# Optimization experiments

Hardware: AMD Instinct MI355X
Metric: run time of the kernel (lower is better)

## Reference

```python
import jax, jax.numpy as jnp
import numpy as np
from jax import lax

DISP = 4   # max displacement for correlation -> 81 channels
KSZ = 3    # deform/gate conv kernel size


def conv2d(x, w, b=None):
    out = lax.conv_general_dilated(x, w, (1, 1), 'SAME',
                                   dimension_numbers=('NCHW', 'OIHW', 'NCHW'))
    if b is not None:
        out = out + b[None, :, None, None]
    return out


def correlation(x1, x2, d=DISP):
    # FlowNet-style cost volume, kernel_size=1: per-displacement channel-mean dot product.
    B, C, H, W = x1.shape
    x2p = jnp.pad(x2, ((0, 0), (0, 0), (d, d), (d, d)))
    outs = []
    for dy in range(2 * d + 1):
        for dx in range(2 * d + 1):
            shifted = lax.dynamic_slice(x2p, (0, 0, dy, dx), (B, C, H, W))
            outs.append(jnp.sum(x1 * shifted, axis=1) / C)
    return jnp.stack(outs, axis=1)  # [B, (2d+1)^2, H, W]


def bilinear_sample(img, y, x):
    # img: [B,C,H,W]; y,x: [B,H,W] float sample coords; zero padding outside.
    B, C, H, W = img.shape
    y0 = jnp.floor(y); x0 = jnp.floor(x)
    y1 = y0 + 1.0;     x1 = x0 + 1.0
    wy1 = y - y0; wx1 = x - x0
    wy0 = 1.0 - wy1; wx0 = 1.0 - wx1
    flat = img.reshape(B, C, H * W)

    def gather(yi, xi):
        valid = (yi >= 0) & (yi <= H - 1) & (xi >= 0) & (xi <= W - 1)
        yc = jnp.clip(yi, 0, H - 1).astype(jnp.int32)
        xc = jnp.clip(xi, 0, W - 1).astype(jnp.int32)
        idx = (yc * W + xc).reshape(B, 1, H * W)
        g = jnp.take_along_axis(flat, idx, axis=2).reshape(B, C, H, W)
        return g * valid.astype(img.dtype)[:, None]

    return (gather(y0, x0) * (wy0 * wx0)[:, None]
          + gather(y0, x1) * (wy0 * wx1)[:, None]
          + gather(y1, x0) * (wy1 * wx0)[:, None]
          + gather(y1, x1) * (wy1 * wx1)[:, None])


def deform_conv(img, offset, w, k=KSZ):
    # offset: [B, 2*k*k, H, W] with (dy, dx) pairs per kernel tap (row-major).
    B, C, H, W = img.shape
    pad = (k - 1) // 2
    ys = jnp.arange(H, dtype=img.dtype)[None, :, None]
    xs = jnp.arange(W, dtype=img.dtype)[None, None, :]
    out = jnp.zeros((B, w.shape[0], H, W), dtype=img.dtype)
    for kk in range(k * k):
        ky, kx = kk // k, kk % k
        y = ys + (ky - pad) + offset[:, 2 * kk]
        x = xs + (kx - pad) + offset[:, 2 * kk + 1]
        s = bilinear_sample(img, y, x)
        out = out + jnp.einsum('oc,bchw->bohw', w[:, :, ky, kx], s)
    return out


def linear_scale(x, std_multiplier=3.0):
    pos = x > 0
    cnt = jnp.sum(pos).astype(x.dtype)
    mean = jnp.sum(jnp.where(pos, x, 0.0)) / jnp.maximum(cnt, 1.0)
    var = jnp.sum(jnp.where(pos, (x - mean) ** 2, 0.0)) / jnp.maximum(cnt - 1.0, 1.0)
    ub = mean + std_multiplier * jnp.sqrt(var)
    ub = jnp.where(cnt >= 2.0, ub, 1.0)  # matches torch nan / empty-positive fallback
    return jnp.clip(x, 0.0, lax.stop_gradient(ub)) / ub


def setup_inputs() -> dict:
    key = jax.random.key(0)
    ks = jax.random.split(key, 10)
    B, C, H, W = 8, 256, 64, 64
    f = jnp.float32
    inp = {
        'inputs':   jax.random.normal(ks[0], (B, C, H, W), f),
        'in_state': jax.random.normal(ks[1], (B, C, H, W), f),
        'w_reset':  jax.random.normal(ks[2], (C, 2 * C, 3, 3), f) * 0.02,
        'b_reset':  jnp.zeros((C,), f),
        'w_update': jax.random.normal(ks[3], (C, 2 * C, 3, 3), f) * 0.02,
        'b_update': jnp.zeros((C,), f),
        'w_out':    jax.random.normal(ks[4], (C, 2 * C, 3, 3), f) * 0.02,
        'b_out':    jnp.zeros((C,), f),
        'w_offset': jax.random.normal(ks[5], (18, 81, 1, 1), f) * 0.01,
        'w_align':  jax.random.normal(ks[6], (C, C, 3, 3), f) * 0.01,
    }
    return inp


def reference(inputs, in_state, w_reset, b_reset, w_update, b_update,
              w_out, b_out, w_offset, w_align):
    # align_features: correlation -> 1x1 offset conv -> deformable conv
    corr = correlation(inputs, in_state)
    offset = conv2d(corr, w_offset)
    aligned = deform_conv(in_state, offset, w_align)
    # ConvGRU gates with linear-scaled relu gates
    stacked = jnp.concatenate([inputs, aligned], axis=1)
    update = linear_scale(jax.nn.relu(conv2d(stacked, w_update, b_update)))
    reset = linear_scale(jax.nn.relu(conv2d(stacked, w_reset, b_reset)))
    out_in = jax.nn.relu(conv2d(jnp.concatenate([inputs, in_state * reset], axis=1), w_out, b_out))
    new_state = in_state * (1.0 - update) + out_in * update
    return (new_state, new_state)  # (out_feat, new_state)
```

## Files before the change

### kernel.cpp

```cpp
#include <hip/hip_runtime.h>
#include <stdint.h>
#include <math.h>

typedef unsigned short u16;
typedef short bf16x8 __attribute__((ext_vector_type(8)));
typedef float f32x4 __attribute__((ext_vector_type(4)));

#define MFMA16x16x32(a,b,c) __builtin_amdgcn_mfma_f32_16x16x32_bf16((a),(b),(c),0,0,0)

typedef __attribute__((address_space(3))) void as3_void;
typedef const __attribute__((address_space(1))) void as1_void;

__device__ __forceinline__ void g2l16(const void* g, void* l){
#if __has_builtin(__builtin_amdgcn_global_load_lds)
  __builtin_amdgcn_global_load_lds((as1_void*)g, (as3_void*)l, 16, 0, 0);
#else
  *(int4*)l = *(const int4*)g;
#endif
}

__device__ __forceinline__ u16 f2bf(float f){
  uint32_t u = __builtin_bit_cast(uint32_t, f);
  u += 0x7fffu + ((u >> 16) & 1u);
  return (u16)(u >> 16);
}
__device__ __forceinline__ float bf2f(u16 h){
  uint32_t u = ((uint32_t)h) << 16;
  return __builtin_bit_cast(float, u);
}
__device__ __forceinline__ void unpack8(int4 v, float* o){
  uint32_t w0=(uint32_t)v.x, w1=(uint32_t)v.y, w2=(uint32_t)v.z, w3=(uint32_t)v.w;
  o[0]=__builtin_bit_cast(float, w0<<16); o[1]=__builtin_bit_cast(float, w0&0xffff0000u);
  o[2]=__builtin_bit_cast(float, w1<<16); o[3]=__builtin_bit_cast(float, w1&0xffff0000u);
  o[4]=__builtin_bit_cast(float, w2<<16); o[5]=__builtin_bit_cast(float, w2&0xffff0000u);
  o[6]=__builtin_bit_cast(float, w3<<16); o[7]=__builtin_bit_cast(float, w3&0xffff0000u);
}
__device__ __forceinline__ int iclampi(int v,int lo,int hi){ return v<lo?lo:(v>hi?hi:v); }

__global__ void k_repack(const float* __restrict__ w_reset, const float* __restrict__ b_reset,
                         const float* __restrict__ w_update, const float* __restrict__ b_update,
                         const float* __restrict__ w_out, const float* __restrict__ w_offset,
                         const float* __restrict__ w_align,
                         u16* __restrict__ wgate, u16* __restrict__ wout,
                         u16* __restrict__ walign, float* __restrict__ woff,
                         float* __restrict__ biascat){
  int idx = blockIdx.x * 256 + threadIdx.x;
  if (idx < 512*4608){
    int e = idx & 7, j = (idx >> 3) & 2047, chunk = idx >> 14;
    int nb = chunk & 1, kk = chunk >> 1;
    int l = j & 15, q = (j >> 4) & 3, t16 = (j >> 6) & 15, ks2 = j >> 10;
    int n = nb*256 + t16*16 + l;
    int tap = kk >> 3, ksin = kk & 7;
    int c = ksin*64 + ks2*32 + q*8 + e;
    int ky = tap/3, kx = tap%3;
    float v = (n < 256) ? w_update[((n*512 + c)*3 + ky)*3 + kx]
                        : w_reset[(((n-256)*512 + c)*3 + ky)*3 + kx];
    wgate[idx] = f2bf(v);
  }
  if (idx < 256*4608){
    int e = idx & 7, j = (idx >> 3) & 1023, chunk = idx >> 13;
    int nb = chunk & 1, kk = chunk >> 1;
    int l = j & 15, q = (j >> 4) & 3, t8 = (j >> 6) & 7, ks2 = j >> 9;
    int n = nb*128 + t8*16 + l;
    int tap = kk >> 3, ksin = kk & 7;
    int c = ksin*64 + ks2*32 + q*8 + e;
    int ky = tap/3, kx = tap%3;
    wout[idx] = f2bf(w_out[((n*512 + c)*3 + ky)*3 + kx]);
  }
  if (idx < 256*2304){
    int n = idx / 2304, k = idx % 2304;
    int tap = k >> 8, c = k & 255;
    int ky = tap/3, kx = tap%3;
    walign[idx] = f2bf(w_align[((n*256 + c)*3 + ky)*3 + kx]);
  }
  if (idx < 1458) woff[idx] = w_offset[idx] * (1.f/256.f);
  if (idx < 512) biascat[idx] = (idx < 256) ? b_update[idx] : b_reset[idx-256];
}

__global__ __launch_bounds__(256) void k_transform(const float* __restrict__ inputs,
    const float* __restrict__ in_state, u16* __restrict__ stacked,
    u16* __restrict__ stacked2, u16* __restrict__ x2pad){
  __shared__ u16 t1[64*264];
  __shared__ u16 t2[64*264];
  int tid = threadIdx.x, bh = blockIdx.x;
  int b = bh >> 6, h = bh & 63;
  int w = tid & 63, cq = tid >> 6;
  for (int i = 0; i < 64; ++i){
    int c = i*4 + cq;
    int gi = ((b*256 + c)*64 + h)*64 + w;
    t1[w*264 + c] = f2bf(inputs[gi]);
    t2[w*264 + c] = f2bf(in_state[gi]);
  }
  __syncthreads();
  int px = tid >> 2, cg = tid & 3;
#pragma unroll
  for (int u = 0; u < 8; ++u){
    int c = cg*64 + u*8;
    int4 v1 = *(const int4*)(t1 + px*264 + c);
    int4 v2 = *(const int4*)(t2 + px*264 + c);
    *(int4*)(stacked  + (((b*66 + h+1)*66) + (px+1))*512 + c) = v1;
    *(int4*)(stacked2 + (((b*66 + h+1)*66) + (px+1))*512 + c) = v1;
    *(int4*)(x2pad    + (((b*72 + h+4)*72) + (px+4))*256 + c) = v2;
  }
}

__global__ __launch_bounds__(256) void k_corr(const u16* __restrict__ stacked,
    const u16* __restrict__ x2pad, float* __restrict__ corr){
  __shared__ u16 lA[8192];
  __shared__ u16 lB[32768];
  int tid = threadIdx.x, idx = blockIdx.x;
  int b = idx >> 6, ty = (idx >> 3) & 7, tx = idx & 7;
  int h0 = ty*8, w0 = tx*8;
  int wave = tid >> 6, lane = tid & 63, l15 = lane & 15, quad = lane >> 4;
  f32x4 acc[4][4];
#pragma unroll
  for (int i=0;i<4;i++)
#pragma unroll
    for (int j=0;j<4;j++){ f32x4 z = {0.f,0.f,0.f,0.f}; acc[i][j] = z; }

  for (int s = 0; s < 2; ++s){
#pragma unroll
    for (int i = 0; i < 4; ++i){
      int j = tid + i*256;
      int ml = j & 15, q = (j>>4)&3, mt = (j>>6)&3, ks = j >> 8;
      int px = mt*16 + ml, py = px >> 3, pxx = px & 7;
      const u16* g = stacked + (((b*66 + h0+py+1)*66) + (w0+pxx+1))*512 + s*128 + ks*32 + q*8;
      g2l16(g, lA + j*8);
    }
#pragma unroll
    for (int i = 0; i < 16; ++i){
      int j = tid + i*256;
      int nl = j & 15, q = (j>>4)&3, nt = (j>>6)&15, ks = j >> 10;
      int qp = nt*16 + nl, qy = qp >> 4, qx = qp & 15;
      const u16* g = x2pad + (((b*72 + h0+qy)*72) + (w0+qx))*256 + s*128 + ks*32 + q*8;
      g2l16(g, lB + j*8);
    }
    __syncthreads();
#pragma unroll
    for (int ks = 0; ks < 4; ++ks){
      bf16x8 bv[4];
#pragma unroll
      for (int ni=0; ni<4; ++ni){
        int nt = wave*4 + ni;
        bv[ni] = *(const bf16x8*)(lB + (((ks*16 + nt)*4 + quad)*16 + l15)*8);
      }
#pragma unroll
      for (int mi=0; mi<4; ++mi){
        bf16x8 av = *(const bf16x8*)(lA + (((ks*4 + mi)*4 + quad)*16 + l15)*8);
#pragma unroll
        for (int ni=0; ni<4; ++ni) acc[mi][ni] = MFMA16x16x32(av, bv[ni], acc[mi][ni]);
      }
    }
    __syncthreads();
  }
#pragma unroll
  for (int mi=0; mi<4; ++mi){
#pragma unroll
    for (int ni=0; ni<4; ++ni){
      int n = wave*64 + ni*16 + l15;
      int qy = n >> 4, qx = n & 15;
#pragma unroll
      for (int r=0; r<4; ++r){
        int m = mi*16 + quad*4 + r;
        int py = m >> 3, pxx = m & 7;
        int dy = qy - py, dx = qx - pxx;
        if ((unsigned)dy <= 8u && (unsigned)dx <= 8u)
          corr[(((b*64 + h0+py)*64) + (w0+pxx))*81 + dy*9 + dx] = acc[mi][ni][r];
      }
    }
  }
}

__global__ __launch_bounds__(256) void k_offset(const float* __restrict__ corr,
    const float* __restrict__ woff, float* __restrict__ offs){
  __shared__ float lc[32*84];
  __shared__ float lw[18*84];
  int tid = threadIdx.x, blk = blockIdx.x;
  int row = blk >> 1, half = blk & 1;
  int base = row*5184 + half*32*81;
  for (int i = tid; i < 32*81; i += 256){
    int px = i / 81, d = i % 81;
    lc[px*84 + d] = corr[base + i];
  }
  for (int i = tid; i < 18*84; i += 256){
    int o = i / 84, d = i % 84;
    if (d < 81) lw[i] = woff[o*81 + d];
  }
  __syncthreads();
  int px = tid & 31, og = tid >> 5;
  for (int o = og; o < 18; o += 8){
    float s = 0.f;
#pragma unroll
    for (int dd = 0; dd < 20; ++dd){
      float4 a = *(const float4*)(lc + px*84 + dd*4);
      float4 wv = *(const float4*)(lw + o*84 + dd*4);
      s += a.x*wv.x + a.y*wv.y + a.z*wv.z + a.w*wv.w;
    }
    s += lc[px*84 + 80] * lw[o*84 + 80];
    offs[(row*64 + half*32 + px)*18 + o] = s;
  }
}

__global__ __launch_bounds__(256) void k_deform(const u16* __restrict__ x2pad,
    const float* __restrict__ offs, const u16* __restrict__ walign,
    u16* __restrict__ stacked){
  __shared__ u16 lA[16384];
  int tid = threadIdx.x, bh = blockIdx.x;
  int b = bh >> 6, h = bh & 63;
  int wave = tid >> 6, lane = tid & 63, l15 = lane & 15, quad = lane >> 4;
  int px = tid >> 2, cg = tid & 3;
  int mt_s = px >> 4, ml_s = px & 15;
  f32x4 acc[4][4];
#pragma unroll
  for (int i=0;i<4;i++)
#pragma unroll
    for (int j=0;j<4;j++){ f32x4 z = {0.f,0.f,0.f,0.f}; acc[i][j] = z; }

  for (int tap = 0; tap < 9; ++tap){
    int ky = tap/3, kx = tap%3;
    float offy = offs[(bh*64 + px)*18 + 2*tap];
    float offx = offs[(bh*64 + px)*18 + 2*tap + 1];
    float y = (float)(h + ky - 1) + offy;
    float x = (float)(px + kx - 1) + offx;
    float y0f = floorf(y), x0f = floorf(x);
    float wy1 = y - y0f, wx1 = x - x0f;
    float wy0 = 1.f - wy1, wx0 = 1.f - wx1;
    int iy0 = iclampi((int)y0f, -4, 67), ix0 = iclampi((int)x0f, -4, 67);
    int iy1 = iclampi((int)y0f + 1, -4, 67), ix1 = iclampi((int)x0f + 1, -4, 67);
    const u16* p00 = x2pad + (((b*72 + iy0+4)*72) + (ix0+4))*256 + cg*64;
    const u16* p01 = x2pad + (((b*72 + iy0+4)*72) + (ix1+4))*256 + cg*64;
    const u16* p10 = x2pad + (((b*72 + iy1+4)*72) + (ix0+4))*256 + cg*64;
    const u16* p11 = x2pad + (((b*72 + iy1+4)*72) + (ix1+4))*256 + cg*64;
    float w00 = wy0*wx0, w01 = wy0*wx1, w10 = wy1*wx0, w11 = wy1*wx1;
#pragma unroll
    for (int u = 0; u < 8; ++u){
      int4 v00 = *(const int4*)(p00 + u*8);
      int4 v01 = *(const int4*)(p01 + u*8);
      int4 v10 = *(const int4*)(p10 + u*8);
      int4 v11 = *(const int4*)(p11 + u*8);
      float a00[8], a01[8], a10[8], a11[8];
      unpack8(v00,a00); unpack8(v01,a01); unpack8(v10,a10); unpack8(v11,a11);
      union { u16 h2[8]; int4 v; } R;
#pragma unroll
      for (int jj = 0; jj < 8; ++jj)
        R.h2[jj] = f2bf(w00*a00[jj] + w01*a01[jj] + w10*a10[jj] + w11*a11[jj]);
      int ch = cg*64 + u*8;
      int ks = ch >> 5, q = (ch >> 3) & 3;
      *(int4*)(lA + (((ks*4 + mt_s)*4 + q)*16 + ml_s)*8) = R.v;
    }
    __syncthreads();
#pragma unroll
    for (int ks = 0; ks < 8; ++ks){
      bf16x8 bv[4];
#pragma unroll
      for (int ni=0; ni<4; ++ni){
        int n = wave*64 + ni*16 + l15;
        bv[ni] = *(const bf16x8*)(walign + n*2304 + tap*256 + ks*32 + quad*8);
      }
#pragma unroll
      for (int mi=0; mi<4; ++mi){
        bf16x8 av = *(const bf16x8*)(lA + (((ks*4 + mi)*4 + quad)*16 + l15)*8);
#pragma unroll
        for (int ni=0; ni<4; ++ni) acc[mi][ni] = MFMA16x16x32(av, bv[ni], acc[mi][ni]);
      }
    }
    __syncthreads();
  }
#pragma unroll
  for (int mi=0; mi<4; ++mi){
#pragma unroll
    for (int ni=0; ni<4; ++ni){
      int n = wave*64 + ni*16 + l15;
#pragma unroll
      for (int r=0; r<4; ++r){
        int m = mi*16 + quad*4 + r;
        stacked[(((b*66 + h+1)*66) + (m+1))*512 + 256 + n] = f2bf(acc[mi][ni][r]);
      }
    }
  }
}

__device__ __forceinline__ void stageA_k(u16* __restrict__ dst,
    const u16* __restrict__ in, int b, int h0, int kk, int ks2, int tid){
  int tap = kk >> 3, ksin = kk & 7;
  int ky = tap/3, kx = tap - ky*3;
  const u16* abase = in + ((b*66 + h0 + ky)*66 + kx)*512 + ksin*64 + ks2*32;
#pragma unroll
  for (int i = 0; i < 2; ++i){
    int j = (ks2<<10) | (i<<9) | tid;
    int l = j & 15, q = (j >> 4) & 3, t16 = (j >> 6) & 15;
    int px = t16*16 + l, r = px >> 6, w = px & 63;
    g2l16(abase + (r*66 + w)*512 + q*8, dst + j*8);
  }
}
__device__ __forceinline__ void stageB16_k(u16* __restrict__ dst,
    const u16* __restrict__ wts, int nb, int kk, int ks2, int tid){
  const u16* wch = wts + (size_t)(kk*2 + nb) * 16384;
#pragma unroll
  for (int i = 0; i < 2; ++i){
    int j = (ks2<<10) | (i<<9) | tid;
    g2l16(wch + j*8, dst + j*8);
  }
}
__device__ __forceinline__ void stageB8_k(u16* __restrict__ dst,
    const u16* __restrict__ wts, int nb, int kk, int ks2, int tid){
  const u16* wch = wts + (size_t)(kk*2 + nb) * 8192;
  int j = (ks2<<9) | tid;
  g2l16(wch + j*8, dst + j*8);
}

#define PHASE16(MH, K2, LOADB, STG_STMT, WV) do { \
  bf16x8 av_[4]; \
  _Pragma("unroll") \
  for (int m4=0;m4<4;++m4) \
    av_[m4] = *(const bf16x8*)(Acur + ((((K2)*16 + wm*8 + (MH)*4 + m4)*4 + quad)*16 + l15)*8); \
  if constexpr (LOADB){ \
    _Pragma("unroll") \
    for (int ni=0;ni<4;++ni) \
      bv_[ni] = *(const bf16x8*)(Bcur + ((((K2)*16 + wn*4 + ni)*4 + quad)*16 + l15)*8); \
  } \
  STG_STMT; \
  asm volatile("" ::: "memory"); \
  __builtin_amdgcn_s_barrier(); \
  asm volatile("s_waitcnt lgkmcnt(0)" ::: "memory"); \
  __builtin_amdgcn_sched_barrier(0); \
  __builtin_amdgcn_s_setprio(1); \
  _Pragma("unroll") \
  for (int m4=0;m4<4;++m4){ \
    _Pragma("unroll") \
    for (int ni=0;ni<4;++ni) \
      acc[(MH)*4+m4][ni] = MFMA16x16x32(av_[m4], bv_[ni], acc[(MH)*4+m4][ni]); \
  } \
  __builtin_amdgcn_s_setprio(0); \
  __builtin_amdgcn_sched_barrier(0); \
  if ((WV) >= 0){ \
    if (hasnext) { asm volatile("s_waitcnt vmcnt(%0)" :: "i"((WV) < 0 ? 0 : (WV)) : "memory"); } \
    else         { asm volatile("s_waitcnt vmcnt(0)" ::: "memory"); } \
  } \
  asm volatile("" ::: "memory"); \
  __builtin_amdgcn_s_barrier(); \
} while(0)

#define PHASE8(K2, STG_STMT, WV) do { \
  bf16x8 av_[8]; \
  _Pragma("unroll") \
  for (int m8=0;m8<8;++m8) \
    av_[m8] = *(const bf16x8*)(Acur + ((((K2)*16 + wm*8 + m8)*4 + quad)*16 + l15)*8); \
  _Pragma("unroll") \
  for (int ni=0;ni<2;++ni) \
    bv_[ni] = *(const bf16x8*)(Bcur + ((((K2)*8 + wn*2 + ni)*4 + quad)*16 + l15)*8); \
  STG_STMT; \
  asm volatile("" ::: "memory"); \
  __builtin_amdgcn_s_barrier(); \
  asm volatile("s_waitcnt lgkmcnt(0)" ::: "memory"); \
  __builtin_amdgcn_sched_barrier(0); \
  __builtin_amdgcn_s_setprio(1); \
  _Pragma("unroll") \
  for (int m8=0;m8<8;++m8){ \
    _Pragma("unroll") \
    for (int ni=0;ni<2;++ni) \
      acc[m8][ni] = MFMA16x16x32(av_[m8], bv_[ni], acc[m8][ni]); \
  } \
  __builtin_amdgcn_s_setprio(0); \
  __builtin_amdgcn_sched_barrier(0); \
  if (hasnext) { asm volatile("s_waitcnt vmcnt(%0)" :: "i"(WV) : "memory"); } \
  else         { asm volatile("s_waitcnt vmcnt(0)" ::: "memory"); } \
  asm volatile("" ::: "memory"); \
  __builtin_amdgcn_s_barrier(); \
} while(0)

template<int NT, bool STATS>
__global__ __launch_bounds__(512, 2) void k_conv256(const u16* __restrict__ in,
    const u16* __restrict__ wts, const float* __restrict__ bias,
    u16* __restrict__ outp, float* __restrict__ partials){
  constexpr int NI = NT / 4;
  __shared__ u16 lA[2][16384];
  __shared__ u16 lB[2][NT*1024];

  int tid = threadIdx.x, g = blockIdx.x;
  int work = (g & 7) * 32 + (g >> 3);
  int nb = work >> 7, mt = work & 127;
  int b = mt >> 4, h0 = (mt & 15) * 4;
  int wave = tid >> 6, lane = tid & 63, l15 = lane & 15, quad = lane >> 4;
  int wm = wave & 1, wn = wave >> 1;

  f32x4 acc[8][NI];
#pragma unroll
  for (int i=0;i<8;i++)
#pragma unroll
    for (int j=0;j<NI;j++){ f32x4 z = {0.f,0.f,0.f,0.f}; acc[i][j] = z; }

  if constexpr (NT == 16){
    stageA_k(&lA[0][0], in, b, h0, 0, 0, tid);
    stageB16_k(&lB[0][0], wts, nb, 0, 0, tid);
    stageA_k(&lA[0][0], in, b, h0, 0, 1, tid);
    stageB16_k(&lB[0][0], wts, nb, 0, 1, tid);
    asm volatile("s_waitcnt vmcnt(4)" ::: "memory");
  } else {
    stageA_k(&lA[0][0], in, b, h0, 0, 0, tid);
    stageB8_k(&lB[0][0], wts, nb, 0, 0, tid);
    stageA_k(&lA[0][0], in, b, h0, 0, 1, tid);
    stageB8_k(&lB[0][0], wts, nb, 0, 1, tid);
    asm volatile("s_waitcnt vmcnt(3)" ::: "memory");
  }
  asm volatile("" ::: "memory");
  __builtin_amdgcn_s_barrier();

#pragma unroll 1
  for (int t = 0; t < 72; ++t){
    int d = t & 1;
    const u16* Acur = &lA[d][0];
    const u16* Bcur = &lB[d][0];
    u16* Anext = &lA[d^1][0];
    u16* Bnext = &lB[d^1][0];
    bool hasnext = (t < 71);
    int kn = t + 1;
    if constexpr (NT == 16){
      bf16x8 bv_[4];
      PHASE16(0, 0, 1, if (hasnext) stageA_k(Anext, in, b, h0, kn, 0, tid), -1);
      PHASE16(1, 0, 0, if (hasnext) stageB16_k(Bnext, wts, nb, kn, 0, tid), 4);
      PHASE16(0, 1, 1, if (hasnext) stageA_k(Anext, in, b, h0, kn, 1, tid), -1);
      PHASE16(1, 1, 0, if (hasnext) stageB16_k(Bnext, wts, nb, kn, 1, tid), 4);
    } else {
      bf16x8 bv_[2];
      PHASE8(0, if (hasnext){ stageA_k(Anext, in, b, h0, kn, 0, tid);
                              stageB8_k(Bnext, wts, nb, kn, 0, tid); }, 3);
      PHASE8(1, if (hasnext){ stageA_k(Anext, in, b, h0, kn, 1, tid);
                              stageB8_k(Bnext, wts, nb, kn, 1, tid); }, 3);
    }
  }

  float bvl[NI];
#pragma unroll
  for (int ni = 0; ni < NI; ++ni)
    bvl[ni] = bias[nb*(NT*16) + wn*(NI*16) + ni*16 + l15];
  float sc = 0.f, ss = 0.f, sq = 0.f;
#pragma unroll
  for (int mi=0; mi<8; ++mi){
#pragma unroll
    for (int ni=0; ni<NI; ++ni){
      int n = nb*(NT*16) + wn*(NI*16) + ni*16 + l15;
#pragma unroll
      for (int r=0; r<4; ++r){
        int m = wm*128 + mi*16 + quad*4 + r;
        int row = h0 + (m >> 6), w = m & 63;
        float v = acc[mi][ni][r] + bvl[ni];
        v = fmaxf(v, 0.f);
        outp[(((b*64 + row)*64) + w)*(NT*32) + n] = f2bf(v);
        if (STATS){ sc += (v > 0.f) ? 1.f : 0.f; ss += v; sq += v*v; }
      }
    }
  }
  if constexpr (STATS){
    __shared__ float red[8][3];
#pragma unroll
    for (int off = 32; off; off >>= 1){
      sc += __shfl_down(sc, off); ss += __shfl_down(ss, off); sq += __shfl_down(sq, off);
    }
    if (lane == 0){ red[wave][0]=sc; red[wave][1]=ss; red[wave][2]=sq; }
    __syncthreads();
    if (tid == 0){
      float a0=0,a1=0,a2=0;
      for (int w2=0; w2<8; ++w2){ a0+=red[w2][0]; a1+=red[w2][1]; a2+=red[w2][2]; }
      partials[work*3+0]=a0; partials[work*3+1]=a1; partials[work*3+2]=a2;
    }
  }
}

__global__ __launch_bounds__(256) void k_finalize(const float* __restrict__ partials,
                                                  float* __restrict__ ubs){
  __shared__ float red[4][6];
  int tid = threadIdx.x, lane = tid & 63, wave = tid >> 6;
  float cu=0,su=0,qu=0,cr=0,sr=0,qr=0;
  {
    float c = partials[tid*3+0], s = partials[tid*3+1], q = partials[tid*3+2];
    if (tid < 128){ cu=c; su=s; qu=q; } else { cr=c; sr=s; qr=q; }
  }
#pragma unroll
  for (int off = 32; off; off >>= 1){
    cu += __shfl_down(cu, off); su += __shfl_down(su, off); qu += __shfl_down(qu, off);
    cr += __shfl_down(cr, off); sr += __shfl_down(sr, off); qr += __shfl_down(qr, off);
  }
  if (lane == 0){ red[wave][0]=cu; red[wave][1]=su; red[wave][2]=qu;
                  red[wave][3]=cr; red[wave][4]=sr; red[wave][5]=qr; }
  __syncthreads();
  if (tid < 2){
    double C=0, S=0, Q=0;
    for (int w2=0; w2<4; ++w2){
      C += red[w2][tid*3+0]; S += red[w2][tid*3+1]; Q += red[w2][tid*3+2];
    }
    float ub = 1.f;
    if (C >= 2.0){
      double mean = S / C;
      double var = (Q - C*mean*mean) / (C - 1.0);
      if (var < 0.0) var = 0.0;
      ub = (float)(mean + 3.0*sqrt(var));
    }
    ubs[tid] = ub;
    ubs[2+tid] = 1.f/ub;
  }
}

__global__ __launch_bounds__(256) void k_mulreset(const u16* __restrict__ G,
    const u16* __restrict__ x2pad, const float* __restrict__ ubs,
    u16* __restrict__ stacked2){
  int tid = threadIdx.x, bh = blockIdx.x;
  int b = bh >> 6, h = bh & 63;
  int px = tid >> 2, cg = tid & 3;
  float ubr = ubs[1], inv = ubs[3];
#pragma unroll
  for (int u = 0; u < 8; ++u){
    int c = cg*64 + u*8;
    int4 gv = *(const int4*)(G + (bh*64 + px)*512 + 256 + c);
    int4 sv = *(const int4*)(x2pad + (((b*72 + h+4)*72) + (px+4))*256 + c);
    float gf[8], sf[8]; unpack8(gv, gf); unpack8(sv, sf);
    union { u16 h2[8]; int4 v; } R;
#pragma unroll
    for (int j=0;j<8;j++){
      float r = fminf(gf[j], ubr) * inv;
      R.h2[j] = f2bf(sf[j] * r);
    }
    *(int4*)(stacked2 + (((b*66 + h+1)*66) + (px+1))*512 + 256 + c) = R.v;
  }
}

__global__ __launch_bounds__(256) void k_final(const u16* __restrict__ G,
    const u16* __restrict__ O, const float* __restrict__ in_state,
    const float* __restrict__ ubs, float* __restrict__ dout){
  __shared__ float Q[64*65];
  __shared__ float P[64*65];
  int tid = threadIdx.x, bh = blockIdx.x;
  int b = bh >> 6, h = bh & 63;
  float ubu = ubs[0], inv = ubs[2];
  int px = tid >> 2, cs = (tid & 3)*16;
  int w = tid & 63, c4 = tid >> 6;
  for (int cb = 0; cb < 4; ++cb){
#pragma unroll
    for (int tt = 0; tt < 2; ++tt){
      int cl = cs + tt*8;
      int c = cb*64 + cl;
      int4 gv = *(const int4*)(G + (bh*64 + px)*512 + c);
      int4 ov = *(const int4*)(O + (bh*64 + px)*256 + c);
      float gf[8], of[8]; unpack8(gv, gf); unpack8(ov, of);
#pragma unroll
      for (int j=0;j<8;j++){
        float u = fminf(gf[j], ubu) * inv;
        Q[px*65 + cl + j] = u;
        P[px*65 + cl + j] = of[j]*u;
      }
    }
    __syncthreads();
    for (int i = 0; i < 16; ++i){
      int cl = i*4 + c4;
      int c = cb*64 + cl;
      int gidx = (((b*256 + c)*64) + h)*64 + w;
      float s = in_state[gidx];
      float v = s*(1.f - Q[w*65 + cl]) + P[w*65 + cl];
      dout[gidx] = v;
      dout[8388608 + gidx] = v;
    }
    __syncthreads();
  }
}

extern "C" void kernel_launch(void* const* d_in, const int* in_sizes, int n_in,
                              void* d_out, int out_size, void* d_ws, size_t ws_size,
                              hipStream_t stream){
  (void)in_sizes; (void)n_in; (void)out_size; (void)ws_size;
  const float* inputs   = (const float*)d_in[0];
  const float* in_state = (const float*)d_in[1];
  const float* w_reset  = (const float*)d_in[2];
  const float* b_reset  = (const float*)d_in[3];
  const float* w_update = (const float*)d_in[4];
  const float* b_update = (const float*)d_in[5];
  const float* w_out    = (const float*)d_in[6];
  const float* b_out    = (const float*)d_in[7];
  const float* w_offset = (const float*)d_in[8];
  const float* w_align  = (const float*)d_in[9];
  float* dout = (float*)d_out;

  char* ws = (char*)d_ws;
  size_t off = 0;
  auto alloc = [&](size_t bytes)->char*{
    char* p = ws + off; off = (off + bytes + 255) & ~(size_t)255; return p;
  };
  const size_t x2pad_b   = 8ull*72*72*256*2;
  const size_t stacked_b = 8ull*66*66*512*2;
  u16* x2pad    = (u16*)alloc(x2pad_b);
  u16* stacked  = (u16*)alloc(stacked_b);
  u16* stacked2 = (u16*)alloc(stacked_b);
  float* corr   = (float*)alloc(8ull*64*64*81*4);
  float* offs   = (float*)alloc(8ull*64*64*18*4);
  u16* G        = (u16*)alloc(8ull*64*64*512*2);
  u16* O        = (u16*)alloc(8ull*64*64*256*2);
  u16* wgate    = (u16*)alloc(512ull*4608*2);
  u16* woutb    = (u16*)alloc(256ull*4608*2);
  u16* walignb  = (u16*)alloc(256ull*2304*2);
  float* woff   = (float*)alloc(1458*4);
  float* biascat= (float*)alloc(512*4);
  float* partials=(float*)alloc(1024*3*4);
  float* ubs    = (float*)alloc(4*4);

  hipMemsetAsync(x2pad,    0, x2pad_b,   stream);
  hipMemsetAsync(stacked,  0, stacked_b, stream);
  hipMemsetAsync(stacked2, 0, stacked_b, stream);

  k_repack<<<9216, 256, 0, stream>>>(w_reset, b_reset, w_update, b_update, w_out,
                                     w_offset, w_align, wgate, woutb, walignb, woff, biascat);
  k_transform<<<512, 256, 0, stream>>>(inputs, in_state, stacked, stacked2, x2pad);
  k_corr<<<512, 256, 0, stream>>>(stacked, x2pad, corr);
  k_offset<<<1024, 256, 0, stream>>>(corr, woff, offs);
  k_deform<<<512, 256, 0, stream>>>(x2pad, offs, walignb, stacked);
  k_conv256<16, true><<<256, 512, 0, stream>>>(stacked, wgate, biascat, G, partials);
  k_finalize<<<1, 256, 0, stream>>>(partials, ubs);
  k_mulreset<<<512, 256, 0, stream>>>(G, x2pad, ubs, stacked2);
  k_conv256<8, false><<<256, 512, 0, stream>>>(stacked2, woutb, b_out, O, nullptr);
  k_final<<<512, 256, 0, stream>>>(G, O, in_state, ubs, dout);
}
```

Before: 669.4 us.

## Software-pipeline LDS fragment reads with register double-buffering in conv GEMM loop

```diff
diff --git a/kernel.cpp b/kernel.cpp
--- a/kernel.cpp
+++ b/kernel.cpp
@@ -309,65 +309,57 @@
   g2l16(wch + j*8, dst + j*8);
 }
 
-#define PHASE16(MH, K2, LOADB, STG_STMT, WV) do { \
-  bf16x8 av_[4]; \
+#define PH16(CMH, AVC, BVC, AVN, BVN, LOADB, RA, RB, NMH, NK2, STG, EPI) do { \
   _Pragma("unroll") \
-  for (int m4=0;m4<4;++m4) \
-    av_[m4] = *(const bf16x8*)(Acur + ((((K2)*16 + wm*8 + (MH)*4 + m4)*4 + quad)*16 + l15)*8); \
-  if constexpr (LOADB){ \
+  for (int m4_=0;m4_<4;++m4_) \
+    AVN[m4_] = *(const bf16x8*)((const u16*)(RA) + ((((NK2)*16 + wm*8 + (NMH)*4 + m4_)*4 + quad)*16 + l15)*8); \
+  if (LOADB){ \
     _Pragma("unroll") \
-    for (int ni=0;ni<4;++ni) \
-      bv_[ni] = *(const bf16x8*)(Bcur + ((((K2)*16 + wn*4 + ni)*4 + quad)*16 + l15)*8); \
+    for (int ni_=0;ni_<4;++ni_) \
+      BVN[ni_] = *(const bf16x8*)((const u16*)(RB) + ((((NK2)*16 + wn*4 + ni_)*4 + quad)*16 + l15)*8); \
   } \
-  STG_STMT; \
-  asm volatile("" ::: "memory"); \
-  __builtin_amdgcn_s_barrier(); \
-  asm volatile("s_waitcnt lgkmcnt(0)" ::: "memory"); \
+  STG; \
   __builtin_amdgcn_sched_barrier(0); \
   __builtin_amdgcn_s_setprio(1); \
   _Pragma("unroll") \
-  for (int m4=0;m4<4;++m4){ \
+  for (int m4_=0;m4_<4;++m4_){ \
     _Pragma("unroll") \
-    for (int ni=0;ni<4;++ni) \
-      acc[(MH)*4+m4][ni] = MFMA16x16x32(av_[m4], bv_[ni], acc[(MH)*4+m4][ni]); \
+    for (int ni_=0;ni_<4;++ni_) \
+      acc[(CMH)*4+m4_][ni_] = MFMA16x16x32(AVC[m4_], BVC[ni_], acc[(CMH)*4+m4_][ni_]); \
   } \
   __builtin_amdgcn_s_setprio(0); \
   __builtin_amdgcn_sched_barrier(0); \
-  if ((WV) >= 0){ \
-    if (hasnext) { asm volatile("s_waitcnt vmcnt(%0)" :: "i"((WV) < 0 ? 0 : (WV)) : "memory"); } \
-    else         { asm volatile("s_waitcnt vmcnt(0)" ::: "memory"); } \
+  EPI; \
+} while(0)
+
+#define PH8(AVC, BVC, AVN, BVN, RA, RB, NK2, STG, EPI) do { \
+  _Pragma("unroll") \
+  for (int m8_=0;m8_<8;++m8_) \
+    AVN[m8_] = *(const bf16x8*)((const u16*)(RA) + ((((NK2)*16 + wm*8 + m8_)*4 + quad)*16 + l15)*8); \
+  _Pragma("unroll") \
+  for (int ni_=0;ni_<2;++ni_) \
+    BVN[ni_] = *(const bf16x8*)((const u16*)(RB) + ((((NK2)*8 + wn*2 + ni_)*4 + quad)*16 + l15)*8); \
+  STG; \
+  __builtin_amdgcn_sched_barrier(0); \
+  __builtin_amdgcn_s_setprio(1); \
+  _Pragma("unroll") \
+  for (int m8_=0;m8_<8;++m8_){ \
+    _Pragma("unroll") \
+    for (int ni_=0;ni_<2;++ni_) \
+      acc[m8_][ni_] = MFMA16x16x32(AVC[m8_], BVC[ni_], acc[m8_][ni_]); \
   } \
+  __builtin_amdgcn_s_setprio(0); \
+  __builtin_amdgcn_sched_barrier(0); \
+  EPI; \
+} while(0)
+
+#define VMBAR(N) do { \
+  if (N) { asm volatile("s_waitcnt vmcnt(" #N ")" ::: "memory"); } \
+  else   { asm volatile("s_waitcnt vmcnt(0)" ::: "memory"); } \
   asm volatile("" ::: "memory"); \
   __builtin_amdgcn_s_barrier(); \
 } while(0)
-
-#define PHASE8(K2, STG_STMT, WV) do { \
-  bf16x8 av_[8]; \
-  _Pragma("unroll") \
-  for (int m8=0;m8<8;++m8) \
-    av_[m8] = *(const bf16x8*)(Acur + ((((K2)*16 + wm*8 + m8)*4 + quad)*16 + l15)*8); \
-  _Pragma("unroll") \
-  for (int ni=0;ni<2;++ni) \
-    bv_[ni] = *(const bf16x8*)(Bcur + ((((K2)*8 + wn*2 + ni)*4 + quad)*16 + l15)*8); \
-  STG_STMT; \
-  asm volatile("" ::: "memory"); \
-  __builtin_amdgcn_s_barrier(); \
-  asm volatile("s_waitcnt lgkmcnt(0)" ::: "memory"); \
-  __builtin_amdgcn_sched_barrier(0); \
-  __builtin_amdgcn_s_setprio(1); \
-  _Pragma("unroll") \
-  for (int m8=0;m8<8;++m8){ \
-    _Pragma("unroll") \
-    for (int ni=0;ni<2;++ni) \
-      acc[m8][ni] = MFMA16x16x32(av_[m8], bv_[ni], acc[m8][ni]); \
-  } \
-  __builtin_amdgcn_s_setprio(0); \
-  __builtin_amdgcn_sched_barrier(0); \
-  if (hasnext) { asm volatile("s_waitcnt vmcnt(%0)" :: "i"(WV) : "memory"); } \
-  else         { asm volatile("s_waitcnt vmcnt(0)" ::: "memory"); } \
-  asm volatile("" ::: "memory"); \
-  __builtin_amdgcn_s_barrier(); \
-} while(0)
+#define BARONLY do { asm volatile("" ::: "memory"); __builtin_amdgcn_s_barrier(); } while(0)
 
 template<int NT, bool STATS>
 __global__ __launch_bounds__(512, 2) void k_conv256(const u16* __restrict__ in,
@@ -391,42 +383,78 @@
     for (int j=0;j<NI;j++){ f32x4 z = {0.f,0.f,0.f,0.f}; acc[i][j] = z; }
 
   if constexpr (NT == 16){
+    bf16x8 avA[4], avB[4], bvA[4], bvB[4];
     stageA_k(&lA[0][0], in, b, h0, 0, 0, tid);
     stageB16_k(&lB[0][0], wts, nb, 0, 0, tid);
     stageA_k(&lA[0][0], in, b, h0, 0, 1, tid);
     stageB16_k(&lB[0][0], wts, nb, 0, 1, tid);
     asm volatile("s_waitcnt vmcnt(4)" ::: "memory");
+    asm volatile("" ::: "memory");
+    __builtin_amdgcn_s_barrier();
+#pragma unroll
+    for (int m4_=0;m4_<4;++m4_)
+      avA[m4_] = *(const bf16x8*)(&lA[0][0] + (((wm*8 + m4_)*4 + quad)*16 + l15)*8);
+#pragma unroll
+    for (int ni_=0;ni_<4;++ni_)
+      bvA[ni_] = *(const bf16x8*)(&lB[0][0] + (((wn*4 + ni_)*4 + quad)*16 + l15)*8);
+
+#pragma unroll 1
+    for (int t = 0; t < 72; ++t){
+      int d = t & 1;
+      const u16* Acur = &lA[d][0];
+      const u16* Bcur = &lB[d][0];
+      u16* Anx = &lA[d^1][0];
+      u16* Bnx = &lB[d^1][0];
+      bool hn = (t < 71);
+      int kn = t + 1;
+      PH16(0, avA, bvA, avB, bvB, 0, Acur, Bcur, 1, 0,
+           if (hn){ stageA_k(Anx, in, b, h0, kn, 0, tid);
+                    stageB16_k(Bnx, wts, nb, kn, 0, tid); },
+           if (hn) VMBAR(4); else VMBAR(0));
+      PH16(1, avB, bvA, avA, bvB, 1, Acur, Bcur, 0, 1, , );
+      PH16(0, avA, bvB, avB, bvA, 0, Acur, Bcur, 1, 1,
+           if (hn){ stageA_k(Anx, in, b, h0, kn, 1, tid);
+                    stageB16_k(Bnx, wts, nb, kn, 1, tid); },
+           if (hn) VMBAR(4); else VMBAR(0));
+      PH16(1, avB, bvB, avA, bvA, 1, Anx, Bnx, 0, 0, , BARONLY);
+    }
   } else {
+    bf16x8 avA[8], avB[8], bvA[2], bvB[2];
     stageA_k(&lA[0][0], in, b, h0, 0, 0, tid);
     stageB8_k(&lB[0][0], wts, nb, 0, 0, tid);
     stageA_k(&lA[0][0], in, b, h0, 0, 1, tid);
     stageB8_k(&lB[0][0], wts, nb, 0, 1, tid);
+    stageA_k(&lA[1][0], in, b, h0, 1, 0, tid);
+    stageB8_k(&lB[1][0], wts, nb, 1, 0, tid);
     asm volatile("s_waitcnt vmcnt(3)" ::: "memory");
-  }
-  asm volatile("" ::: "memory");
-  __builtin_amdgcn_s_barrier();
+    asm volatile("" ::: "memory");
+    __builtin_amdgcn_s_barrier();
+#pragma unroll
+    for (int m8_=0;m8_<8;++m8_)
+      avA[m8_] = *(const bf16x8*)(&lA[0][0] + (((wm*8 + m8_)*4 + quad)*16 + l15)*8);
+#pragma unroll
+    for (int ni_=0;ni_<2;++ni_)
+      bvA[ni_] = *(const bf16x8*)(&lB[0][0] + (((wn*2 + ni_)*4 + quad)*16 + l15)*8);
 
 #pragma unroll 1
-  for (int t = 0; t < 72; ++t){
-    int d = t & 1;
-    const u16* Acur = &lA[d][0];
-    const u16* Bcur = &lB[d][0];
-    u16* Anext = &lA[d^1][0];
-    u16* Bnext = &lB[d^1][0];
-    bool hasnext = (t < 71);
-    int kn = t + 1;
-    if constexpr (NT == 16){
-      bf16x8 bv_[4];
-      PHASE16(0, 0, 1, if (hasnext) stageA_k(Anext, in, b, h0, kn, 0, tid), -1);
-      PHASE16(1, 0, 0, if (hasnext) stageB16_k(Bnext, wts, nb, kn, 0, tid), 4);
-      PHASE16(0, 1, 1, if (hasnext) stageA_k(Anext, in, b, h0, kn, 1, tid), -1);
-      PHASE16(1, 1, 0, if (hasnext) stageB16_k(Bnext, wts, nb, kn, 1, tid), 4);
-    } else {
-      bf16x8 bv_[2];
-      PHASE8(0, if (hasnext){ stageA_k(Anext, in, b, h0, kn, 0, tid);
-                              stageB8_k(Bnext, wts, nb, kn, 0, tid); }, 3);
-      PHASE8(1, if (hasnext){ stageA_k(Anext, in, b, h0, kn, 1, tid);
-                              stageB8_k(Bnext, wts, nb, kn, 1, tid); }, 3);
+    for (int t = 0; t < 72; ++t){
+      int d = t & 1;
+      const u16* Acur = &lA[d][0];
+      const u16* Bcur = &lB[d][0];
+      u16* Anx = &lA[d^1][0];
+      u16* Bnx = &lB[d^1][0];
+      u16* Acu = &lA[d][0];
+      u16* Bcu = &lB[d][0];
+      bool h1 = (t < 71), h2 = (t < 70);
+      int kn = t + 1;
+      PH8(avA, bvA, avB, bvB, Acur, Bcur, 1,
+          if (h1){ stageA_k(Anx, in, b, h0, kn, 1, tid);
+                   stageB8_k(Bnx, wts, nb, kn, 1, tid); },
+          if (h1) VMBAR(3); else VMBAR(0));
+      PH8(avB, bvB, avA, bvA, Anx, Bnx, 0,
+          if (h2){ stageA_k(Acu, in, b, h0, t+2, 0, tid);
+                   stageB8_k(Bcu, wts, nb, t+2, 0, tid); },
+          if (h2) VMBAR(3); else VMBAR(0));
     }
   }
 
```

Measured after the change: 636.2 us. 1.05x faster.
